# Performance work log

Measured on AMD Instinct MI355X. Metric: run time of the kernel, lower is better.

## Reference

```python
import jax, jax.numpy as jnp
import numpy as np

B, T, D = 8, 1024, 1024
H = 16
ATT_DIM = 1024
VAL_DIM = 1024
SCALE = float((D // H) ** 0.5)  # note: uses input_dim//num_heads, not head dim of attention_dim
EPS = 1e-13


def setup_inputs() -> dict:
    key = jax.random.key(0)
    ks = jax.random.split(key, 6)
    inputs = jax.random.normal(ks[0], (B, T, D), dtype=jnp.float32)
    mask = jnp.ones((B, T), dtype=jnp.float32)
    adj = jax.random.uniform(ks[1], (B, T, T), dtype=jnp.float32)
    # combined QKV projection: Linear(D, 2*ATT_DIM + VAL_DIM)
    W_qkv = jax.random.normal(ks[2], (2 * ATT_DIM + VAL_DIM, D), dtype=jnp.float32) * (1.0 / np.sqrt(D))
    b_qkv = jnp.zeros((2 * ATT_DIM + VAL_DIM,), dtype=jnp.float32)
    # output projection: Linear(VAL_DIM, D)
    W_out = jax.random.normal(ks[3], (D, VAL_DIM), dtype=jnp.float32) * (1.0 / np.sqrt(VAL_DIM))
    b_out = jnp.zeros((D,), dtype=jnp.float32)
    return {"inputs": inputs, "mask": mask, "adj": adj,
            "W_qkv": W_qkv, "b_qkv": b_qkv, "W_out": W_out, "b_out": b_out}


def reference(inputs, mask, adj, W_qkv, b_qkv, W_out, b_out):
    b, t, _ = inputs.shape
    dh_a = ATT_DIM // H
    dh_v = VAL_DIM // H
    proj = jnp.einsum('btd,od->bto', inputs, W_qkv) + b_qkv
    q = proj[..., :ATT_DIM]
    k = proj[..., ATT_DIM:2 * ATT_DIM]
    v = proj[..., 2 * ATT_DIM:]
    # [B, H, T, dh]
    q = q.reshape(b, t, H, dh_a).transpose(0, 2, 1, 3)
    k = k.reshape(b, t, H, dh_a).transpose(0, 2, 1, 3)
    v = v.reshape(b, t, H, dh_v).transpose(0, 2, 1, 3)
    scores = jnp.einsum('bhqd,bhkd->bhqk', q, k) / SCALE
    # multiplicative adjacency gate, broadcast over heads
    scores = scores * adj[:, None, :, :]
    # old-allennlp masked_softmax: softmax(scores * mask), re-mask, renormalize
    m = mask[:, None, None, :]  # [B,1,1,T]
    attn = jax.nn.softmax(scores * m, axis=-1)
    attn = attn * m
    attn = attn / (attn.sum(axis=-1, keepdims=True) + EPS)
    out = jnp.einsum('bhqk,bhkd->bhqd', attn, v)  # [B,H,T,dh_v]
    out = out.transpose(0, 2, 1, 3).reshape(b, t, VAL_DIM)
    out = jnp.einsum('btv,ov->bto', out, W_out) + b_out
    return out
```

## Files before the change

kernel.cpp:

```cpp
#include <hip/hip_runtime.h>
#include <hip/hip_bf16.h>
#include <cstdint>


using bf16 = __hip_bfloat16;
typedef __attribute__((ext_vector_type(8))) short short8;
typedef __attribute__((ext_vector_type(4))) short short4v;
typedef __attribute__((ext_vector_type(4))) float floatx4;
typedef __attribute__((ext_vector_type(2))) unsigned int uint2v;

#define B_    8
#define T_    1024
#define D_    1024
#define H_    16
#define PROJW 3072

__device__ __forceinline__ void gl2lds16(const void* g, void* l) {
  __builtin_amdgcn_global_load_lds(
      (const __attribute__((address_space(1))) void*)g,
      (__attribute__((address_space(3))) void*)l,
      16, 0, 0);
}

__device__ __forceinline__ unsigned short f2b_bits(float f) {
  return __builtin_bit_cast(unsigned short, __float2bfloat16(f));
}

__device__ __forceinline__ float fast_exp2(float x) {
#if __has_builtin(__builtin_amdgcn_exp2f)
  return __builtin_amdgcn_exp2f(x);
#else
  float r;
  asm("v_exp_f32 %0, %1\ns_nop 0" : "=v"(r) : "v"(x));
  return r;
#endif
}

__global__ __launch_bounds__(256)
void cvt_f32_bf16(const float* __restrict__ src, bf16* __restrict__ dst, int n) {
  int i = (blockIdx.x * 256 + threadIdx.x) * 4;
  if (i < n) {
    floatx4 f = *(const floatx4*)(src + i);
    short4v h;
    h[0] = f2b_bits(f[0]); h[1] = f2b_bits(f[1]);
    h[2] = f2b_bits(f[2]); h[3] = f2b_bits(f[3]);
    *(short4v*)(dst + i) = h;
  }
}

template<int EPI>
__global__ __launch_bounds__(512)
void gemm_bt_bias(const bf16* __restrict__ A, const bf16* __restrict__ Bm,
                  const bf16* __restrict__ bias, void* __restrict__ C0,
                  void* __restrict__ C1, void* __restrict__ C2,
                  int M, int N, int K)
{
  __shared__ __align__(16) unsigned short sA[2][128 * 64];
  __shared__ __align__(16) unsigned short sB[2][128 * 64];

  const int tid  = threadIdx.x;
  const int lane = tid & 63;
  const int wv   = tid >> 6;
  const int quad = lane >> 4;
  const int l16  = lane & 15;
  const int wm   = wv >> 1;
  const int wn   = wv & 1;

  const int gx   = gridDim.x;
  const int nwg  = gx * gridDim.y;
  const int bidl = blockIdx.y * gx + blockIdx.x;
  const int xcd  = bidl & 7;
  const int c    = bidl >> 3;
  const int cpx  = nwg >> 3;
  const int R    = cpx / gx;
  const int nb   = c / (R * 4);
  const int rem  = c % (R * 4);
  const int bm   = xcd * R + (rem >> 2);
  const int bn   = nb * 4 + (rem & 3);

  floatx4 acc[2][4];
#pragma unroll
  for (int i = 0; i < 2; ++i)
#pragma unroll
    for (int j = 0; j < 4; ++j) acc[i][j] = (floatx4){0.f, 0.f, 0.f, 0.f};

  const int o_base = wv * 1024 + lane * 16;
  const bf16* gA[2];
  const bf16* gB[2];
#pragma unroll
  for (int it = 0; it < 2; ++it) {
    int o   = it * 8192 + o_base;
    int row = o >> 7;
    int col = ((o & 127) ^ ((row & 7) << 4)) >> 1;
    gA[it] = A  + (size_t)(bm * 128 + row) * K + col;
    gB[it] = Bm + (size_t)(bn * 128 + row) * K + col;
  }

  const int NT = K >> 6;
#pragma unroll
  for (int it = 0; it < 2; ++it)
    gl2lds16(gA[it], &sA[0][(it * 8192 + wv * 1024) >> 1]);
#pragma unroll
  for (int it = 0; it < 2; ++it)
    gl2lds16(gB[it], &sB[0][(it * 8192 + wv * 1024) >> 1]);

  const int swx = (l16 & 7) << 3;

  for (int t = 0; t < NT; ++t) {
    const int s = t & 1;
    if (t + 1 < NT) {
#pragma unroll
      for (int it = 0; it < 2; ++it)
        gl2lds16(gA[it] + (size_t)(t + 1) * 64, &sA[s ^ 1][(it * 8192 + wv * 1024) >> 1]);
#pragma unroll
      for (int it = 0; it < 2; ++it)
        gl2lds16(gB[it] + (size_t)(t + 1) * 64, &sB[s ^ 1][(it * 8192 + wv * 1024) >> 1]);
      __builtin_amdgcn_sched_barrier(0);
      asm volatile("s_waitcnt vmcnt(4)" ::: "memory");
    } else {
      asm volatile("s_waitcnt vmcnt(0)" ::: "memory");
    }
    __builtin_amdgcn_s_barrier();
    __builtin_amdgcn_sched_barrier(0);

#pragma unroll
    for (int kk = 0; kk < 64; kk += 32) {
      short8 a_[2], b_[4];
#pragma unroll
      for (int i = 0; i < 2; ++i)
        a_[i] = *(const short8*)&sA[s][(wm * 32 + i * 16 + l16) * 64 + ((kk + quad * 8) ^ swx)];
#pragma unroll
      for (int j = 0; j < 4; ++j)
        b_[j] = *(const short8*)&sB[s][(wn * 64 + j * 16 + l16) * 64 + ((kk + quad * 8) ^ swx)];
#pragma unroll
      for (int i = 0; i < 2; ++i)
#pragma unroll
        for (int j = 0; j < 4; ++j)
          acc[i][j] = __builtin_amdgcn_mfma_f32_16x16x32_bf16(a_[i], b_[j], acc[i][j], 0, 0, 0);
    }

    __builtin_amdgcn_sched_barrier(0);
    __builtin_amdgcn_s_barrier();
  }

  if (EPI == 1) {
#pragma unroll
    for (int j = 0; j < 4; ++j) {
      const int colg = bn * 128 + wn * 64 + j * 16 + l16;
      const float bv = __bfloat162float(bias[colg]);
#pragma unroll
      for (int i = 0; i < 2; ++i)
#pragma unroll
        for (int r = 0; r < 4; ++r) {
          int rowg = bm * 128 + wm * 32 + i * 16 + quad * 4 + r;
          ((float*)C0)[(size_t)rowg * N + colg] = acc[i][j][r] + bv;
        }
    }
  } else {
    const int region = bn >> 3;
    if (region < 2) {
      bf16* dst = (bf16*)(region == 0 ? C0 : C1);
#pragma unroll
      for (int j = 0; j < 4; ++j) {
        const int colg = bn * 128 + wn * 64 + j * 16 + l16;
        const int colr = colg & 1023;
        const float bv = __bfloat162float(bias[colg]);
#pragma unroll
        for (int i = 0; i < 2; ++i)
#pragma unroll
          for (int r = 0; r < 4; ++r) {
            int rowg = bm * 128 + wm * 32 + i * 16 + quad * 4 + r;
            dst[(size_t)rowg * 1024 + colr] = __float2bfloat16(acc[i][j][r] + bv);
          }
      }
    } else {
      bf16* vt = (bf16*)C2;
#pragma unroll
      for (int j = 0; j < 4; ++j) {
        const int colg = bn * 128 + wn * 64 + j * 16 + l16;
        const int d  = colg & 63;
        const int hh = (colg >> 6) & 15;
        const float bv = __bfloat162float(bias[colg]);
#pragma unroll
        for (int i = 0; i < 2; ++i) {
          int rowg0 = bm * 128 + wm * 32 + i * 16 + quad * 4;
          int bb = rowg0 >> 10, t0 = rowg0 & 1023;
          short4v pk;
#pragma unroll
          for (int r = 0; r < 4; ++r) pk[r] = (short)f2b_bits(acc[i][j][r] + bv);
          *(short4v*)&vt[((size_t)(bb * 16 + hh) << 16) + ((size_t)d << 10) + t0] = pk;
        }
      }
    }
  }
}

__global__ __launch_bounds__(512)
void attn_fused(const bf16* __restrict__ Qp, const bf16* __restrict__ Kp,
                const bf16* __restrict__ Vt, const float* __restrict__ adj,
                const float* __restrict__ mask, bf16* __restrict__ aout)
{
  __shared__ __align__(16) unsigned short sK[64 * 72];
  __shared__ __align__(16) unsigned short sVT[64 * 72];
  __shared__ __align__(16) unsigned short sP[128 * 72];

  const int tid  = threadIdx.x;
  const int lane = tid & 63;
  const int wv   = tid >> 6;
  const int quad = lane >> 4;
  const int l16  = lane & 15;

  const int bid  = blockIdx.x + 16 * (blockIdx.y + 8 * blockIdx.z);
  const int b    = bid & 7;
  const int slot = bid >> 3;
  const int h    = slot & 15;
  const int qt   = slot >> 4;

  const bf16* qbase = Qp + (size_t)(b * T_ + qt * 128 + wv * 16 + l16) * 1024 + h * 64 + quad * 8;
  const short8 aq0 = *(const short8*)qbase;
  const short8 aq1 = *(const short8*)(qbase + 32);

  const int srow  = tid >> 3;
  const int chunk = (tid & 7) * 8;
  const int sig = ((srow & 15) << 2) | (srow >> 4);
  const bf16* kb = Kp + (size_t)(b * T_ + sig) * 1024 + h * 64 + chunk;
  const bf16* vb = Vt + ((size_t)(b * 16 + h) << 16) + ((size_t)srow << 10) + chunk;

  const float* mb = mask + b * T_ + l16 * 4;
  const float* adjr[4];
#pragma unroll
  for (int r = 0; r < 4; ++r)
    adjr[r] = adj + ((size_t)b * T_ + qt * 128 + wv * 16 + quad * 4 + r) * T_ + l16 * 4;

  short8 kr = *(const short8*)kb;
  short8 vr = *(const short8*)vb;

  short8 ones8;
#pragma unroll
  for (int i = 0; i < 8; ++i) ones8[i] = (short)0x3F80;

  floatx4 oacc[4];
#pragma unroll
  for (int d = 0; d < 4; ++d) oacc[d] = (floatx4){0.f, 0.f, 0.f, 0.f};
  floatx4 Lacc = (floatx4){0.f, 0.f, 0.f, 0.f};

  const float SC = 0.125f * 1.44269504088896f;

  for (int kt = 0; kt < 16; ++kt) {
    floatx4 av[4];
    floatx4 mk4 = *(const floatx4*)(mb + kt * 64);
#pragma unroll
    for (int r = 0; r < 4; ++r) av[r] = *(const floatx4*)(adjr[r] + kt * 64);
    floatx4 cjv, offv;
#pragma unroll
    for (int j = 0; j < 4; ++j) {
      cjv[j]  = mk4[j] * SC;
      offv[j] = (mk4[j] == 0.f) ? -1e30f : 0.f;
    }

    __syncthreads();
    *(short8*)&sK [srow * 72 + chunk] = kr;
    *(short8*)&sVT[srow * 72 + chunk] = vr;
    __syncthreads();

    {
      int nk = kt < 15 ? kt + 1 : 15;
      kr = *(const short8*)(kb + ((size_t)nk << 16));
      vr = *(const short8*)(vb + (nk << 6));
    }

    floatx4 sacc[4];
#pragma unroll
    for (int j = 0; j < 4; ++j) sacc[j] = (floatx4){0.f, 0.f, 0.f, 0.f};
    __builtin_amdgcn_s_setprio(1);
#pragma unroll
    for (int kk = 0; kk < 64; kk += 32) {
      short8 aq = kk ? aq1 : aq0;
#pragma unroll
      for (int j = 0; j < 4; ++j) {
        short8 bk = *(const short8*)&sK[(j * 16 + l16) * 72 + kk + quad * 8];
        sacc[j] = __builtin_amdgcn_mfma_f32_16x16x32_bf16(aq, bk, sacc[j], 0, 0, 0);
      }
    }
    __builtin_amdgcn_s_setprio(0);

#pragma unroll
    for (int r = 0; r < 4; ++r) {
      floatx4 avc = av[r] * cjv;
      float p[4];
#pragma unroll
      for (int j = 0; j < 4; ++j) {
        float z = fminf(fmaf(sacc[j][r], avc[j], offv[j]), 100.f);
        p[j] = fast_exp2(z);
      }
      unsigned w0, w1;
      asm("v_cvt_pk_bf16_f32 %0, %1, %2" : "=v"(w0) : "v"(p[0]), "v"(p[1]));
      asm("v_cvt_pk_bf16_f32 %0, %1, %2" : "=v"(w1) : "v"(p[2]), "v"(p[3]));
      uint2v pw; pw[0] = w0; pw[1] = w1;
      *(uint2v*)&sP[(wv * 16 + quad * 4 + r) * 72 + l16 * 4] = pw;
    }

    __asm__ __volatile__("" ::: "memory");

    __builtin_amdgcn_s_setprio(1);
#pragma unroll
    for (int kk = 0; kk < 64; kk += 32) {
      short8 ap = *(const short8*)&sP[(wv * 16 + l16) * 72 + kk + quad * 8];
      Lacc = __builtin_amdgcn_mfma_f32_16x16x32_bf16(ap, ones8, Lacc, 0, 0, 0);
#pragma unroll
      for (int d = 0; d < 4; ++d) {
        short8 bv = *(const short8*)&sVT[(d * 16 + l16) * 72 + kk + quad * 8];
        oacc[d] = __builtin_amdgcn_mfma_f32_16x16x32_bf16(ap, bv, oacc[d], 0, 0, 0);
      }
    }
    __builtin_amdgcn_s_setprio(0);
  }

#pragma unroll
  for (int d = 0; d < 4; ++d) {
#pragma unroll
    for (int r = 0; r < 4; ++r) {
      int qrow = qt * 128 + wv * 16 + quad * 4 + r;
      float val = oacc[d][r] / (Lacc[r] + 1e-13f);
      aout[(size_t)(b * T_ + qrow) * 1024 + h * 64 + d * 16 + l16] = __float2bfloat16(val);
    }
  }
}

extern "C" void kernel_launch(void* const* d_in, const int* in_sizes, int n_in,
                              void* d_out, int out_size, void* d_ws, size_t ws_size,
                              hipStream_t stream) {
  const float* inputs = (const float*)d_in[0];
  const float* mask   = (const float*)d_in[1];
  const float* adj    = (const float*)d_in[2];
  const float* W_qkv  = (const float*)d_in[3];
  const float* b_qkv  = (const float*)d_in[4];
  const float* W_out  = (const float*)d_in[5];
  const float* b_out  = (const float*)d_in[6];

  const size_t SEG = (size_t)8192 * 1024;
  bf16* Qp   = (bf16*)d_ws;
  bf16* Kp   = Qp + SEG;
  bf16* Vt   = Kp + SEG;
  bf16* aout = Vt + SEG;
  bf16* wo_bf = Qp;
  bf16* bo_bf = Qp + (size_t)1024 * 1024;

  bf16* ib_bf = (bf16*)d_out;
  bf16* wq_bf = ib_bf + SEG;
  bf16* bq_bf = wq_bf + (size_t)3072 * 1024;

  dim3 blk(256);
  cvt_f32_bf16<<<dim3(8192 * 1024 / 4 / 256), blk, 0, stream>>>(inputs, ib_bf, 8192 * 1024);
  cvt_f32_bf16<<<dim3(3072 * 1024 / 4 / 256), blk, 0, stream>>>(W_qkv, wq_bf, 3072 * 1024);
  cvt_f32_bf16<<<dim3(3), blk, 0, stream>>>(b_qkv, bq_bf, 3072);
  gemm_bt_bias<2><<<dim3(PROJW / 128, (B_ * T_) / 128), dim3(512), 0, stream>>>(
      ib_bf, wq_bf, bq_bf, Qp, Kp, Vt, B_ * T_, PROJW, D_);
  attn_fused<<<dim3(H_, T_ / 128, B_), dim3(512), 0, stream>>>(Qp, Kp, Vt, adj, mask, aout);
  cvt_f32_bf16<<<dim3(1024 * 1024 / 4 / 256), blk, 0, stream>>>(W_out, wo_bf, 1024 * 1024);
  cvt_f32_bf16<<<dim3(1), blk, 0, stream>>>(b_out, bo_bf, 1024);
  gemm_bt_bias<1><<<dim3(D_ / 128, (B_ * T_) / 128), dim3(512), 0, stream>>>(
      aout, wo_bf, bo_bf, d_out, nullptr, nullptr, B_ * T_, D_, D_);
}
```

Measured before the change: 272.7 us.

## Replace QKV projection GEMM with 256x256-tile 8-phase pipelined kernel

Adds a dedicated QKV projection GEMM that uses 256x256 output tiles, with 8 waves each computing 128x64. The kernel interleaves global-to-LDS staging of the next K-tile in eight sub-phases between MFMA bursts, adding explicit vmcnt waits and priority raising. It also uses an XCD-aware block swizzle. The larger tile raises arithmetic intensity and aims to hide load latency, at the cost of 128 KB of LDS and a large accumulator register footprint, which means one block per CU and a small grid of 384 blocks.

```diff
diff --git a/kernel.cpp b/kernel.cpp
--- a/kernel.cpp
+++ b/kernel.cpp
@@ -48,12 +48,167 @@
   }
 }
 
-template<int EPI>
+#define STAGE_A(T, HALF, SLOT) do {                                            \
+    gl2lds16(pA[HALF][0] + (size_t)(T) * 64, &sA[SLOT][(HALF) * 8192 + lds0]); \
+    gl2lds16(pA[HALF][1] + (size_t)(T) * 64, &sA[SLOT][(HALF) * 8192 + lds1]); \
+  } while (0)
+#define STAGE_B(T, HALF, SLOT) do {                                            \
+    gl2lds16(pB[HALF][0] + (size_t)(T) * 64, &sB[SLOT][(HALF) * 8192 + lds0]); \
+    gl2lds16(pB[HALF][1] + (size_t)(T) * 64, &sB[SLOT][(HALF) * 8192 + lds1]); \
+  } while (0)
+#define VMCNT_T do {                                                           \
+    if (st) asm volatile("s_waitcnt vmcnt(4)" ::: "memory");                   \
+    else    asm volatile("s_waitcnt vmcnt(0)" ::: "memory");                   \
+  } while (0)
+
+#define PHASE(Q, CS, STG, VMW) do {                                            \
+    if ((Q) == 0) {                                                            \
+      _Pragma("unroll")                                                        \
+      for (int nj = 0; nj < 4; ++nj)                                           \
+        _Pragma("unroll")                                                      \
+        for (int kq = 0; kq < 2; ++kq)                                         \
+          breg[nj][kq] = *(const short8*)&sB[CS][boffc + nj * 1024 +           \
+                                                 ((kq * 32 + qoff) ^ swx)];    \
+    }                                                                          \
+    short8 areg[2][2];                                                         \
+    _Pragma("unroll")                                                          \
+    for (int mi2 = 0; mi2 < 2; ++mi2)                                          \
+      _Pragma("unroll")                                                        \
+      for (int kq = 0; kq < 2; ++kq)                                           \
+        areg[mi2][kq] = *(const short8*)&sA[CS][aoffc + ((Q) * 2 + mi2) * 1024 \
+                                                + ((kq * 32 + qoff) ^ swx)];   \
+    STG;                                                                       \
+    __builtin_amdgcn_sched_barrier(0);                                         \
+    __builtin_amdgcn_s_barrier();                                              \
+    asm volatile("s_waitcnt lgkmcnt(0)" ::: "memory");                         \
+    __builtin_amdgcn_sched_barrier(0);                                         \
+    __builtin_amdgcn_s_setprio(1);                                             \
+    _Pragma("unroll")                                                          \
+    for (int kq = 0; kq < 2; ++kq)                                             \
+      _Pragma("unroll")                                                        \
+      for (int mi2 = 0; mi2 < 2; ++mi2)                                        \
+        _Pragma("unroll")                                                      \
+        for (int nj = 0; nj < 4; ++nj)                                         \
+          acc[(Q) * 2 + mi2][nj] = __builtin_amdgcn_mfma_f32_16x16x32_bf16(    \
+              areg[mi2][kq], breg[nj][kq], acc[(Q) * 2 + mi2][nj], 0, 0, 0);   \
+    __builtin_amdgcn_s_setprio(0);                                             \
+    VMW;                                                                       \
+    __builtin_amdgcn_sched_barrier(0);                                         \
+    __builtin_amdgcn_s_barrier();                                              \
+  } while (0)
+
 __global__ __launch_bounds__(512)
-void gemm_bt_bias(const bf16* __restrict__ A, const bf16* __restrict__ Bm,
-                  const bf16* __restrict__ bias, void* __restrict__ C0,
-                  void* __restrict__ C1, void* __restrict__ C2,
-                  int M, int N, int K)
+void gemm_qkv_8phase(const bf16* __restrict__ A, const bf16* __restrict__ Bm,
+                     const bf16* __restrict__ bias, bf16* __restrict__ Qp,
+                     bf16* __restrict__ Kp, bf16* __restrict__ Vt)
+{
+  __shared__ __align__(16) unsigned short sA[2][256 * 64];
+  __shared__ __align__(16) unsigned short sB[2][256 * 64];
+
+  const int tid  = threadIdx.x;
+  const int lane = tid & 63;
+  const int wv   = tid >> 6;
+  const int quad = lane >> 4;
+  const int l16  = lane & 15;
+  const int wm   = wv >> 2;
+  const int wn   = wv & 3;
+
+  const int bidl = blockIdx.y * 12 + blockIdx.x;
+  const int swz  = (bidl & 7) * 48 + (bidl >> 3);
+  const int bm   = swz / 12, bn = swz % 12;
+
+  floatx4 acc[8][4];
+#pragma unroll
+  for (int i = 0; i < 8; ++i)
+#pragma unroll
+    for (int j = 0; j < 4; ++j) acc[i][j] = (floatx4){0.f, 0.f, 0.f, 0.f};
+
+  int row_[2], sc_[2];
+#pragma unroll
+  for (int it = 0; it < 2; ++it) {
+    int o = it * 8192 + wv * 1024 + lane * 16;
+    row_[it] = o >> 7;
+    sc_[it]  = ((o & 127) ^ ((row_[it] & 7) << 4)) >> 1;
+  }
+  const bf16* pA[2][2];
+  const bf16* pB[2][2];
+#pragma unroll
+  for (int h = 0; h < 2; ++h)
+#pragma unroll
+    for (int it = 0; it < 2; ++it) {
+      pA[h][it] = A  + (size_t)(bm * 256 + h * 128 + row_[it]) * 1024 + sc_[it];
+      pB[h][it] = Bm + (size_t)(bn * 256 + h * 128 + row_[it]) * 1024 + sc_[it];
+    }
+  const int lds0 = wv * 512;
+  const int lds1 = 4096 + wv * 512;
+
+  const int qoff  = quad * 8;
+  const int swx   = (l16 & 7) << 3;
+  const int aoffc = wm * 8192 + l16 * 64;
+  const int boffc = (wn >> 1) * 8192 + ((wn & 1) * 64 + l16) * 64;
+
+  short8 breg[4][2];
+
+  STAGE_A(0, 0, 0); STAGE_A(0, 1, 0);
+  STAGE_B(0, 0, 0); STAGE_B(0, 1, 0);
+  STAGE_B(1, 0, 1); STAGE_B(1, 1, 1);
+  asm volatile("s_waitcnt vmcnt(4)" ::: "memory");
+  __builtin_amdgcn_s_barrier();
+
+#pragma unroll 1
+  for (int i = 0; i < 8; ++i) {
+    const int t0 = 2 * i;
+    const bool st = (i < 7);
+    PHASE(0, 0, STAGE_A(t0 + 1, 0, 1), (void)0);
+    PHASE(1, 0, STAGE_A(t0 + 1, 1, 1), (void)0);
+    PHASE(2, 0, if (st) STAGE_B(t0 + 2, 0, 0), (void)0);
+    PHASE(3, 0, if (st) STAGE_B(t0 + 2, 1, 0), VMCNT_T);
+    PHASE(0, 1, if (st) STAGE_A(t0 + 2, 0, 0), (void)0);
+    PHASE(1, 1, if (st) STAGE_A(t0 + 2, 1, 0), (void)0);
+    PHASE(2, 1, if (st) STAGE_B(t0 + 3, 0, 1), (void)0);
+    PHASE(3, 1, if (st) STAGE_B(t0 + 3, 1, 1), VMCNT_T);
+  }
+
+  const int region = bn >> 2;
+  if (region < 2) {
+    bf16* dst = region == 0 ? Qp : Kp;
+#pragma unroll
+    for (int nj = 0; nj < 4; ++nj) {
+      const int colg = bn * 256 + wn * 64 + nj * 16 + l16;
+      const int colr = colg & 1023;
+      const float bv = __bfloat162float(bias[colg]);
+#pragma unroll
+      for (int mi = 0; mi < 8; ++mi)
+#pragma unroll
+        for (int r = 0; r < 4; ++r) {
+          int rowg = bm * 256 + wm * 128 + mi * 16 + quad * 4 + r;
+          dst[(size_t)rowg * 1024 + colr] = __float2bfloat16(acc[mi][nj][r] + bv);
+        }
+    }
+  } else {
+#pragma unroll
+    for (int nj = 0; nj < 4; ++nj) {
+      const int colg = bn * 256 + wn * 64 + nj * 16 + l16;
+      const int d  = colg & 63;
+      const int hh = (colg >> 6) & 15;
+      const float bv = __bfloat162float(bias[colg]);
+#pragma unroll
+      for (int mi = 0; mi < 8; ++mi) {
+        int rowg0 = bm * 256 + wm * 128 + mi * 16 + quad * 4;
+        int bb = rowg0 >> 10, t0v = rowg0 & 1023;
+        short4v pk;
+#pragma unroll
+        for (int r = 0; r < 4; ++r) pk[r] = (short)f2b_bits(acc[mi][nj][r] + bv);
+        *(short4v*)&Vt[((size_t)(bb * 16 + hh) << 16) + ((size_t)d << 10) + t0v] = pk;
+      }
+    }
+  }
+}
+
+__global__ __launch_bounds__(512)
+void gemm_bt_bias_f32(const bf16* __restrict__ A, const bf16* __restrict__ Bm,
+                      const bf16* __restrict__ bias, float* __restrict__ C0,
+                      int M, int N, int K)
 {
   __shared__ __align__(16) unsigned short sA[2][128 * 64];
   __shared__ __align__(16) unsigned short sB[2][128 * 64];
@@ -143,55 +298,17 @@
     __builtin_amdgcn_s_barrier();
   }
 
-  if (EPI == 1) {
-#pragma unroll
-    for (int j = 0; j < 4; ++j) {
-      const int colg = bn * 128 + wn * 64 + j * 16 + l16;
-      const float bv = __bfloat162float(bias[colg]);
-#pragma unroll
-      for (int i = 0; i < 2; ++i)
-#pragma unroll
-        for (int r = 0; r < 4; ++r) {
-          int rowg = bm * 128 + wm * 32 + i * 16 + quad * 4 + r;
-          ((float*)C0)[(size_t)rowg * N + colg] = acc[i][j][r] + bv;
-        }
-    }
-  } else {
-    const int region = bn >> 3;
-    if (region < 2) {
-      bf16* dst = (bf16*)(region == 0 ? C0 : C1);
-#pragma unroll
-      for (int j = 0; j < 4; ++j) {
-        const int colg = bn * 128 + wn * 64 + j * 16 + l16;
-        const int colr = colg & 1023;
-        const float bv = __bfloat162float(bias[colg]);
-#pragma unroll
-        for (int i = 0; i < 2; ++i)
-#pragma unroll
-          for (int r = 0; r < 4; ++r) {
-            int rowg = bm * 128 + wm * 32 + i * 16 + quad * 4 + r;
-            dst[(size_t)rowg * 1024 + colr] = __float2bfloat16(acc[i][j][r] + bv);
-          }
+#pragma unroll
+  for (int j = 0; j < 4; ++j) {
+    const int colg = bn * 128 + wn * 64 + j * 16 + l16;
+    const float bv = __bfloat162float(bias[colg]);
+#pragma unroll
+    for (int i = 0; i < 2; ++i)
+#pragma unroll
+      for (int r = 0; r < 4; ++r) {
+        int rowg = bm * 128 + wm * 32 + i * 16 + quad * 4 + r;
+        C0[(size_t)rowg * N + colg] = acc[i][j][r] + bv;
       }
-    } else {
-      bf16* vt = (bf16*)C2;
-#pragma unroll
-      for (int j = 0; j < 4; ++j) {
-        const int colg = bn * 128 + wn * 64 + j * 16 + l16;
-        const int d  = colg & 63;
-        const int hh = (colg >> 6) & 15;
-        const float bv = __bfloat162float(bias[colg]);
-#pragma unroll
-        for (int i = 0; i < 2; ++i) {
-          int rowg0 = bm * 128 + wm * 32 + i * 16 + quad * 4;
-          int bb = rowg0 >> 10, t0 = rowg0 & 1023;
-          short4v pk;
-#pragma unroll
-          for (int r = 0; r < 4; ++r) pk[r] = (short)f2b_bits(acc[i][j][r] + bv);
-          *(short4v*)&vt[((size_t)(bb * 16 + hh) << 16) + ((size_t)d << 10) + t0] = pk;
-        }
-      }
-    }
   }
 }
 
@@ -354,11 +471,11 @@
   cvt_f32_bf16<<<dim3(8192 * 1024 / 4 / 256), blk, 0, stream>>>(inputs, ib_bf, 8192 * 1024);
   cvt_f32_bf16<<<dim3(3072 * 1024 / 4 / 256), blk, 0, stream>>>(W_qkv, wq_bf, 3072 * 1024);
   cvt_f32_bf16<<<dim3(3), blk, 0, stream>>>(b_qkv, bq_bf, 3072);
-  gemm_bt_bias<2><<<dim3(PROJW / 128, (B_ * T_) / 128), dim3(512), 0, stream>>>(
-      ib_bf, wq_bf, bq_bf, Qp, Kp, Vt, B_ * T_, PROJW, D_);
+  gemm_qkv_8phase<<<dim3(PROJW / 256, (B_ * T_) / 256), dim3(512), 0, stream>>>(
+      ib_bf, wq_bf, bq_bf, Qp, Kp, Vt);
   attn_fused<<<dim3(H_, T_ / 128, B_), dim3(512), 0, stream>>>(Qp, Kp, Vt, adj, mask, aout);
   cvt_f32_bf16<<<dim3(1024 * 1024 / 4 / 256), blk, 0, stream>>>(W_out, wo_bf, 1024 * 1024);
   cvt_f32_bf16<<<dim3(1), blk, 0, stream>>>(b_out, bo_bf, 1024);
-  gemm_bt_bias<1><<<dim3(D_ / 128, (B_ * T_) / 128), dim3(512), 0, stream>>>(
-      aout, wo_bf, bo_bf, d_out, nullptr, nullptr, B_ * T_, D_, D_);
-}
+  gemm_bt_bias_f32<<<dim3(D_ / 128, (B_ * T_) / 128), dim3(512), 0, stream>>>(
+      aout, wo_bf, bo_bf, (float*)d_out, B_ * T_, D_, D_);
+}
```

Result: slower. 286.9 us (+5.2%).

## Widen attention key tile to 128 and merge conversion launches, fp32 bias

Applied to the files above, without the earlier changes.

The attention kernel now stages 128 keys per iteration instead of 64. This halves the number of loop iterations and the __syncthreads pairs, and the PV MFMA loop runs over a K=128 tile. The input and W_qkv fp32→bf16 conversions are merged into one launch. The bias conversion kernels are dropped, and the GEMM epilogue reads fp32 bias directly. The larger LDS footprint and the extra prefetch registers may lower occupancy.

```diff
diff --git a/kernel.cpp b/kernel.cpp
--- a/kernel.cpp
+++ b/kernel.cpp
@@ -36,22 +36,32 @@
 #endif
 }
 
+__device__ __forceinline__ void cvt_quad(const float* s, bf16* d, int i) {
+  floatx4 f = *(const floatx4*)(s + i);
+  short4v h;
+  h[0] = f2b_bits(f[0]); h[1] = f2b_bits(f[1]);
+  h[2] = f2b_bits(f[2]); h[3] = f2b_bits(f[3]);
+  *(short4v*)(d + i) = h;
+}
+
 __global__ __launch_bounds__(256)
 void cvt_f32_bf16(const float* __restrict__ src, bf16* __restrict__ dst, int n) {
   int i = (blockIdx.x * 256 + threadIdx.x) * 4;
-  if (i < n) {
-    floatx4 f = *(const floatx4*)(src + i);
-    short4v h;
-    h[0] = f2b_bits(f[0]); h[1] = f2b_bits(f[1]);
-    h[2] = f2b_bits(f[2]); h[3] = f2b_bits(f[3]);
-    *(short4v*)(dst + i) = h;
-  }
+  if (i < n) cvt_quad(src, dst, i);
+}
+
+__global__ __launch_bounds__(256)
+void cvt2_f32_bf16(const float* __restrict__ sa, bf16* __restrict__ da, int nq_a,
+                   const float* __restrict__ sb, bf16* __restrict__ db) {
+  int q = blockIdx.x * 256 + threadIdx.x;
+  if (q < nq_a) cvt_quad(sa, da, q * 4);
+  else          cvt_quad(sb, db, (q - nq_a) * 4);
 }
 
 template<int EPI>
 __global__ __launch_bounds__(512)
 void gemm_bt_bias(const bf16* __restrict__ A, const bf16* __restrict__ Bm,
-                  const bf16* __restrict__ bias, void* __restrict__ C0,
+                  const float* __restrict__ bias, void* __restrict__ C0,
                   void* __restrict__ C1, void* __restrict__ C2,
                   int M, int N, int K)
 {
@@ -147,7 +157,7 @@
 #pragma unroll
     for (int j = 0; j < 4; ++j) {
       const int colg = bn * 128 + wn * 64 + j * 16 + l16;
-      const float bv = __bfloat162float(bias[colg]);
+      const float bv = bias[colg];
 #pragma unroll
       for (int i = 0; i < 2; ++i)
 #pragma unroll
@@ -164,7 +174,7 @@
       for (int j = 0; j < 4; ++j) {
         const int colg = bn * 128 + wn * 64 + j * 16 + l16;
         const int colr = colg & 1023;
-        const float bv = __bfloat162float(bias[colg]);
+        const float bv = bias[colg];
 #pragma unroll
         for (int i = 0; i < 2; ++i)
 #pragma unroll
@@ -180,7 +190,7 @@
         const int colg = bn * 128 + wn * 64 + j * 16 + l16;
         const int d  = colg & 63;
         const int hh = (colg >> 6) & 15;
-        const float bv = __bfloat162float(bias[colg]);
+        const float bv = bias[colg];
 #pragma unroll
         for (int i = 0; i < 2; ++i) {
           int rowg0 = bm * 128 + wm * 32 + i * 16 + quad * 4;
@@ -200,9 +210,9 @@
                 const bf16* __restrict__ Vt, const float* __restrict__ adj,
                 const float* __restrict__ mask, bf16* __restrict__ aout)
 {
-  __shared__ __align__(16) unsigned short sK[64 * 72];
-  __shared__ __align__(16) unsigned short sVT[64 * 72];
-  __shared__ __align__(16) unsigned short sP[128 * 72];
+  __shared__ __align__(16) unsigned short sK [128 * 72];
+  __shared__ __align__(16) unsigned short sVT[64 * 136];
+  __shared__ __align__(16) unsigned short sP [128 * 136];
 
   const int tid  = threadIdx.x;
   const int lane = tid & 63;
@@ -223,8 +233,10 @@
   const int srow  = tid >> 3;
   const int chunk = (tid & 7) * 8;
   const int sig = ((srow & 15) << 2) | (srow >> 4);
-  const bf16* kb = Kp + (size_t)(b * T_ + sig) * 1024 + h * 64 + chunk;
-  const bf16* vb = Vt + ((size_t)(b * 16 + h) << 16) + ((size_t)srow << 10) + chunk;
+  const bf16* kb0 = Kp + (size_t)(b * T_ + sig) * 1024 + h * 64 + chunk;
+  const bf16* kb1 = kb0 + (size_t)64 * 1024;
+  const bf16* vb0 = Vt + ((size_t)(b * 16 + h) << 16) + ((size_t)srow << 10) + chunk;
+  const bf16* vb1 = vb0 + 64;
 
   const float* mb = mask + b * T_ + l16 * 4;
   const float* adjr[4];
@@ -232,8 +244,10 @@
   for (int r = 0; r < 4; ++r)
     adjr[r] = adj + ((size_t)b * T_ + qt * 128 + wv * 16 + quad * 4 + r) * T_ + l16 * 4;
 
-  short8 kr = *(const short8*)kb;
-  short8 vr = *(const short8*)vb;
+  short8 kr0 = *(const short8*)kb0;
+  short8 kr1 = *(const short8*)kb1;
+  short8 vr0 = *(const short8*)vb0;
+  short8 vr1 = *(const short8*)vb1;
 
   short8 ones8;
 #pragma unroll
@@ -246,70 +260,78 @@
 
   const float SC = 0.125f * 1.44269504088896f;
 
-  for (int kt = 0; kt < 16; ++kt) {
-    floatx4 av[4];
-    floatx4 mk4 = *(const floatx4*)(mb + kt * 64);
-#pragma unroll
-    for (int r = 0; r < 4; ++r) av[r] = *(const floatx4*)(adjr[r] + kt * 64);
-    floatx4 cjv, offv;
-#pragma unroll
-    for (int j = 0; j < 4; ++j) {
-      cjv[j]  = mk4[j] * SC;
-      offv[j] = (mk4[j] == 0.f) ? -1e30f : 0.f;
-    }
-
+  for (int kt = 0; kt < 8; ++kt) {
     __syncthreads();
-    *(short8*)&sK [srow * 72 + chunk] = kr;
-    *(short8*)&sVT[srow * 72 + chunk] = vr;
+    *(short8*)&sK [srow * 72 + chunk]        = kr0;
+    *(short8*)&sK [(srow + 64) * 72 + chunk] = kr1;
+    *(short8*)&sVT[srow * 136 + chunk]       = vr0;
+    *(short8*)&sVT[srow * 136 + chunk + 64]  = vr1;
     __syncthreads();
 
     {
-      int nk = kt < 15 ? kt + 1 : 15;
-      kr = *(const short8*)(kb + ((size_t)nk << 16));
-      vr = *(const short8*)(vb + (nk << 6));
-    }
-
-    floatx4 sacc[4];
-#pragma unroll
-    for (int j = 0; j < 4; ++j) sacc[j] = (floatx4){0.f, 0.f, 0.f, 0.f};
+      int nk = kt < 7 ? kt + 1 : 7;
+      kr0 = *(const short8*)(kb0 + ((size_t)nk << 17));
+      kr1 = *(const short8*)(kb1 + ((size_t)nk << 17));
+      vr0 = *(const short8*)(vb0 + (nk << 7));
+      vr1 = *(const short8*)(vb1 + (nk << 7));
+    }
+
+#pragma unroll
+    for (int hh = 0; hh < 2; ++hh) {
+      floatx4 mk4 = *(const floatx4*)(mb + kt * 128 + hh * 64);
+      floatx4 av[4];
+#pragma unroll
+      for (int r = 0; r < 4; ++r)
+        av[r] = *(const floatx4*)(adjr[r] + kt * 128 + hh * 64);
+      floatx4 cjv, offv;
+#pragma unroll
+      for (int j = 0; j < 4; ++j) {
+        cjv[j]  = mk4[j] * SC;
+        offv[j] = (mk4[j] == 0.f) ? -1e30f : 0.f;
+      }
+
+      floatx4 sacc[4];
+#pragma unroll
+      for (int j = 0; j < 4; ++j) sacc[j] = (floatx4){0.f, 0.f, 0.f, 0.f};
+      __builtin_amdgcn_s_setprio(1);
+#pragma unroll
+      for (int kk = 0; kk < 64; kk += 32) {
+        short8 aq = kk ? aq1 : aq0;
+#pragma unroll
+        for (int j = 0; j < 4; ++j) {
+          short8 bk = *(const short8*)&sK[(hh * 64 + j * 16 + l16) * 72 + kk + quad * 8];
+          sacc[j] = __builtin_amdgcn_mfma_f32_16x16x32_bf16(aq, bk, sacc[j], 0, 0, 0);
+        }
+      }
+      __builtin_amdgcn_s_setprio(0);
+
+#pragma unroll
+      for (int r = 0; r < 4; ++r) {
+        floatx4 avc = av[r] * cjv;
+        float p[4];
+#pragma unroll
+        for (int j = 0; j < 4; ++j) {
+          float z = fminf(fmaf(sacc[j][r], avc[j], offv[j]), 100.f);
+          p[j] = fast_exp2(z);
+        }
+        unsigned w0, w1;
+        asm("v_cvt_pk_bf16_f32 %0, %1, %2" : "=v"(w0) : "v"(p[0]), "v"(p[1]));
+        asm("v_cvt_pk_bf16_f32 %0, %1, %2" : "=v"(w1) : "v"(p[2]), "v"(p[3]));
+        uint2v pw; pw[0] = w0; pw[1] = w1;
+        *(uint2v*)&sP[(wv * 16 + quad * 4 + r) * 136 + hh * 64 + l16 * 4] = pw;
+      }
+    }
+
+    __asm__ __volatile__("" ::: "memory");
+
     __builtin_amdgcn_s_setprio(1);
 #pragma unroll
-    for (int kk = 0; kk < 64; kk += 32) {
-      short8 aq = kk ? aq1 : aq0;
-#pragma unroll
-      for (int j = 0; j < 4; ++j) {
-        short8 bk = *(const short8*)&sK[(j * 16 + l16) * 72 + kk + quad * 8];
-        sacc[j] = __builtin_amdgcn_mfma_f32_16x16x32_bf16(aq, bk, sacc[j], 0, 0, 0);
-      }
-    }
-    __builtin_amdgcn_s_setprio(0);
-
-#pragma unroll
-    for (int r = 0; r < 4; ++r) {
-      floatx4 avc = av[r] * cjv;
-      float p[4];
-#pragma unroll
-      for (int j = 0; j < 4; ++j) {
-        float z = fminf(fmaf(sacc[j][r], avc[j], offv[j]), 100.f);
-        p[j] = fast_exp2(z);
-      }
-      unsigned w0, w1;
-      asm("v_cvt_pk_bf16_f32 %0, %1, %2" : "=v"(w0) : "v"(p[0]), "v"(p[1]));
-      asm("v_cvt_pk_bf16_f32 %0, %1, %2" : "=v"(w1) : "v"(p[2]), "v"(p[3]));
-      uint2v pw; pw[0] = w0; pw[1] = w1;
-      *(uint2v*)&sP[(wv * 16 + quad * 4 + r) * 72 + l16 * 4] = pw;
-    }
-
-    __asm__ __volatile__("" ::: "memory");
-
-    __builtin_amdgcn_s_setprio(1);
-#pragma unroll
-    for (int kk = 0; kk < 64; kk += 32) {
-      short8 ap = *(const short8*)&sP[(wv * 16 + l16) * 72 + kk + quad * 8];
+    for (int kk = 0; kk < 128; kk += 32) {
+      short8 ap = *(const short8*)&sP[(wv * 16 + l16) * 136 + kk + quad * 8];
       Lacc = __builtin_amdgcn_mfma_f32_16x16x32_bf16(ap, ones8, Lacc, 0, 0, 0);
 #pragma unroll
       for (int d = 0; d < 4; ++d) {
-        short8 bv = *(const short8*)&sVT[(d * 16 + l16) * 72 + kk + quad * 8];
+        short8 bv = *(const short8*)&sVT[(d * 16 + l16) * 136 + kk + quad * 8];
         oacc[d] = __builtin_amdgcn_mfma_f32_16x16x32_bf16(ap, bv, oacc[d], 0, 0, 0);
       }
     }
@@ -344,21 +366,17 @@
   bf16* Vt   = Kp + SEG;
   bf16* aout = Vt + SEG;
   bf16* wo_bf = Qp;
-  bf16* bo_bf = Qp + (size_t)1024 * 1024;
 
   bf16* ib_bf = (bf16*)d_out;
   bf16* wq_bf = ib_bf + SEG;
-  bf16* bq_bf = wq_bf + (size_t)3072 * 1024;
 
   dim3 blk(256);
-  cvt_f32_bf16<<<dim3(8192 * 1024 / 4 / 256), blk, 0, stream>>>(inputs, ib_bf, 8192 * 1024);
-  cvt_f32_bf16<<<dim3(3072 * 1024 / 4 / 256), blk, 0, stream>>>(W_qkv, wq_bf, 3072 * 1024);
-  cvt_f32_bf16<<<dim3(3), blk, 0, stream>>>(b_qkv, bq_bf, 3072);
+  cvt2_f32_bf16<<<dim3((8192 * 1024 + 3072 * 1024) / 4 / 256), blk, 0, stream>>>(
+      inputs, ib_bf, 8192 * 1024 / 4, W_qkv, wq_bf);
   gemm_bt_bias<2><<<dim3(PROJW / 128, (B_ * T_) / 128), dim3(512), 0, stream>>>(
-      ib_bf, wq_bf, bq_bf, Qp, Kp, Vt, B_ * T_, PROJW, D_);
+      ib_bf, wq_bf, b_qkv, Qp, Kp, Vt, B_ * T_, PROJW, D_);
   attn_fused<<<dim3(H_, T_ / 128, B_), dim3(512), 0, stream>>>(Qp, Kp, Vt, adj, mask, aout);
   cvt_f32_bf16<<<dim3(1024 * 1024 / 4 / 256), blk, 0, stream>>>(W_out, wo_bf, 1024 * 1024);
-  cvt_f32_bf16<<<dim3(1), blk, 0, stream>>>(b_out, bo_bf, 1024);
   gemm_bt_bias<1><<<dim3(D_ / 128, (B_ * T_) / 128), dim3(512), 0, stream>>>(
-      aout, wo_bf, bo_bf, d_out, nullptr, nullptr, B_ * T_, D_, D_);
-}
+      aout, wo_bf, b_out, d_out, nullptr, nullptr, B_ * T_, D_, D_);
+}
```

New measurement: 308.4 us. +13.1%, slower.
